# Performance work log

Hardware: AMD Instinct MI355X
Metric: run time of the kernel (lower is better)

Reference implementation:

```python
import jax, jax.numpy as jnp
import numpy as np

EPS = 1e-3        # Sinkhorn regularization (SinkhornDistance default)
MAX_ITER = 10     # max Sinkhorn iterations
THRESH = 0.1      # early-stop threshold on |u - u_prev|
N, P, D = 8, 2048, 64


def _l2norm(x):
    # F.normalize(x, dim=-1): x / max(||x||_2, 1e-12)
    return x / jnp.maximum(jnp.linalg.norm(x, axis=-1, keepdims=True), 1e-12)


def _l1norm(x):
    # F.normalize(x, p=1, dim=-1)
    return x / jnp.maximum(jnp.sum(jnp.abs(x), axis=-1, keepdims=True), 1e-12)


def _M(C, u, v):
    # modified cost M_ij = (-C_ij + u_i + v_j) / eps
    return (-C + u[..., :, None] + v[..., None, :]) / EPS


def _sinkhorn_uv(C, mu, nu):
    """Log-domain Sinkhorn with early stopping (matches torch loop + err.item() break)."""
    u0 = jnp.zeros_like(mu)
    v0 = jnp.zeros_like(nu)

    def cond(st):
        i, u, v, err = st
        return jnp.logical_and(i < MAX_ITER, err >= THRESH)

    def body(st):
        i, u, v, _ = st
        u1 = u
        u = EPS * (jnp.log(mu + 1e-8) - jax.nn.logsumexp(_M(C, u, v), axis=-1)) + u
        # logsumexp of M^T over last dim == logsumexp of M over axis -2
        v = EPS * (jnp.log(nu + 1e-8) - jax.nn.logsumexp(_M(C, u, v), axis=-2)) + v
        err = jnp.mean(jnp.sum(jnp.abs(u - u1), axis=-1))
        return (i + 1, u, v, err)

    _, u, v, _ = jax.lax.while_loop(
        cond, body, (jnp.int32(0), u0, v0, jnp.float32(jnp.inf)))
    return u, v


def setup_inputs() -> dict:
    key = jax.random.key(0)
    ka, kb = jax.random.split(key)
    a = jax.random.normal(ka, (N, P, D), dtype=jnp.float32)
    b = jax.random.normal(kb, (N, P, D), dtype=jnp.float32)
    return {"a": a, "b": b}


def reference(a, b):
    a = _l2norm(a)
    b = _l2norm(b)
    cost = 1.0 - jnp.einsum('bnd,bmd->bnm', a, b)          # [N, P1, P2]

    # weights computed from detached cost
    Cd = jax.lax.stop_gradient(cost)
    S = 1.0 - Cd
    wa = _l1norm(jnp.clip(_l1norm(jnp.mean(S, axis=2)), 0.0))  # [N, P1]
    wb = _l1norm(jnp.clip(_l1norm(jnp.mean(S, axis=1)), 0.0))  # [N, P2]

    u, v = _sinkhorn_uv(Cd, wa, wb)
    pi = jax.lax.stop_gradient(jnp.exp(_M(Cd, u, v)))       # transport plan, detached
    D_out = jnp.sum(pi * cost, axis=(-2, -1))               # [N], reduction='none'
    return D_out
```

## Files before the change

kernel.cpp:

```cpp
#include <hip/hip_runtime.h>
#include <math.h>

#define NB 8
#define PP 2048
#define DD 64
#define EPSF 1e-3f
#define RCPE 1000.0f
#define TMAX 10
#define THRESHF 0.1f
#define NEG_INF (-1e30f)
#define QSCALE 32767.5f
#define S_DEQ  (1.0f / 32767.5f)
#define KR 512
#define KC 512
#define TSEL 0.15f
#define TSELQ 4915

typedef __attribute__((ext_vector_type(8))) short bf16x8;
typedef __attribute__((ext_vector_type(4))) float f32x4;

__device__ __forceinline__ float waveAllMax(float v) {
#pragma unroll
    for (int m = 1; m < 64; m <<= 1) v = fmaxf(v, __shfl_xor(v, m, 64));
    return v;
}
__device__ __forceinline__ int waveAllMinI(int v) {
#pragma unroll
    for (int m = 1; m < 64; m <<= 1) v = min(v, __shfl_xor(v, m, 64));
    return v;
}
__device__ __forceinline__ float waveAllSum(float v) {
#pragma unroll
    for (int m = 1; m < 64; m <<= 1) v += __shfl_xor(v, m, 64);
    return v;
}
__device__ __forceinline__ short f2bf(float x) {
    unsigned b = __float_as_uint(x);
    return (short)((b + 0x7FFFu + ((b >> 16) & 1u)) >> 16);
}
__device__ __forceinline__ float bf2f(short h) {
    return __uint_as_float(((unsigned)(unsigned short)h) << 16);
}
__device__ __forceinline__ unsigned pknorm_u16(float a, float b) {
    unsigned r;
    asm("v_cvt_pknorm_u16_f32 %0, %1, %2" : "=v"(r) : "v"(a), "v"(b));
    return r;
}

__global__ void norm_kernel(const float* __restrict__ a, const float* __restrict__ b,
                            short* __restrict__ ahi, short* __restrict__ alo,
                            short* __restrict__ bhi, short* __restrict__ blo,
                            float* __restrict__ u, float* __restrict__ v,
                            int* __restrict__ conv, float* __restrict__ out,
                            float* __restrict__ Sa) {
    int gt = blockIdx.x * 256 + threadIdx.x;
    if (gt < NB * PP) { u[gt] = 0.0f; v[gt] = 0.0f; }
    if (gt == 0) *conv = 0;
    if (gt < NB) out[gt] = 0.0f;
    if (gt < 2 * NB * DD) Sa[gt] = 0.0f;
    int wave = gt >> 6;
    int lane = threadIdx.x & 63;
    const float* src; short* dhi; short* dlo; int row;
    if (wave < NB * PP) { src = a; dhi = ahi; dlo = alo; row = wave; }
    else                { src = b; dhi = bhi; dlo = blo; row = wave - NB * PP; }
    float x = src[(size_t)row * DD + lane];
    float ss = waveAllSum(x * x);
    float r = 1.0f / fmaxf(sqrtf(ss), 1e-12f);
    float xn = x * r;
    short h = f2bf(xn);
    dhi[(size_t)row * DD + lane] = h;
    dlo[(size_t)row * DD + lane] = f2bf(xn - bf2f(h));
}

__global__ void sumvec_kernel(const short* __restrict__ ahi, const short* __restrict__ alo,
                              const short* __restrict__ bhi, const short* __restrict__ blo,
                              float* __restrict__ Sa, float* __restrict__ Sb) {
    int b = blockIdx.x >> 3;
    bool isB = (blockIdx.x >> 2) & 1;
    int qtr = blockIdx.x & 3;
    const short* hi = (isB ? bhi : ahi) + ((size_t)b * PP + qtr * 512) * DD;
    const short* lo = (isB ? blo : alo) + ((size_t)b * PP + qtr * 512) * DD;
    float* dst = (isB ? Sb : Sa) + b * DD;
    int t = threadIdx.x;
    int w = t >> 6, lane = t & 63;
    int rl = lane >> 3, dq = lane & 7;
    float s[8] = {};
#pragma unroll
    for (int it = 0; it < 16; ++it) {
        size_t o = (size_t)(w * 128 + it * 8 + rl) * DD + dq * 8;
        bf16x8 h = *(const bf16x8*)(hi + o);
        bf16x8 l = *(const bf16x8*)(lo + o);
#pragma unroll
        for (int e = 0; e < 8; ++e) s[e] += bf2f(h[e]) + bf2f(l[e]);
    }
#pragma unroll
    for (int e = 0; e < 8; ++e) {
#pragma unroll
        for (int m = 8; m < 64; m <<= 1) s[e] += __shfl_xor(s[e], m, 64);
    }
    __shared__ float sh[4][64];
    if (rl == 0) {
#pragma unroll
        for (int e = 0; e < 8; ++e) sh[w][dq * 8 + e] = s[e];
    }
    __syncthreads();
    if (t < 64) atomicAdd(&dst[t], sh[0][t] + sh[1][t] + sh[2][t] + sh[3][t]);
}

__global__ __launch_bounds__(256, 4) void cost_kernel(const short* __restrict__ ahi,
        const short* __restrict__ alo, const short* __restrict__ bhi,
        const short* __restrict__ blo, unsigned short* __restrict__ C16,
        unsigned* __restrict__ rminp, unsigned* __restrict__ cminp) {
    __shared__ short Bs[2][128 * 64];
    __shared__ unsigned cmin2[4][128];
    int b  = blockIdx.z;
    int i0 = blockIdx.y * 128;
    int j0 = blockIdx.x * 128;
    int t = threadIdx.x, w = t >> 6, lane = t & 63;
    int quad = lane >> 4, li = lane & 15;
    const char* bh = (const char*)(bhi + ((size_t)b * PP + j0) * DD);
    const char* bl = (const char*)(blo + ((size_t)b * PP + j0) * DD);
    uint4 st[8];
#pragma unroll
    for (int i = 0; i < 4; ++i) {
        unsigned x = (unsigned)(t + i * 256) * 16;
        unsigned sx = x ^ (((x >> 7) & 7u) << 4);
        st[i]     = *(const uint4*)(bh + sx);
        st[4 + i] = *(const uint4*)(bl + sx);
    }
#pragma unroll
    for (int i = 0; i < 4; ++i) {
        unsigned x = (unsigned)(t + i * 256) * 16;
        *(uint4*)((char*)&Bs[0][0] + x) = st[i];
        *(uint4*)((char*)&Bs[1][0] + x) = st[4 + i];
    }
    __syncthreads();
    size_t Aoff = ((size_t)b * PP + i0 + w * 32) * DD;
    f32x4 acc[2][2][4] = {};
#pragma unroll
    for (int kc = 0; kc < 2; ++kc) {
        int k0 = kc * 32 + quad * 8;
        bf16x8 fah[2], fal[2];
#pragma unroll
        for (int mt = 0; mt < 2; ++mt) {
            size_t o = Aoff + (size_t)(mt * 16 + li) * DD + k0;
            fah[mt] = *(const bf16x8*)(ahi + o);
            fal[mt] = *(const bf16x8*)(alo + o);
        }
#pragma unroll
        for (int nh = 0; nh < 2; ++nh) {
#pragma unroll
            for (int ntl = 0; ntl < 4; ++ntl) {
                int col = nh * 64 + li * 4 + ntl;
                unsigned xo = ((unsigned)col * 128 + (unsigned)(kc * 4 + quad) * 16)
                              ^ (((unsigned)col & 7u) << 4);
                bf16x8 fbh = *(const bf16x8*)((const char*)&Bs[0][0] + xo);
                bf16x8 fbl = *(const bf16x8*)((const char*)&Bs[1][0] + xo);
#pragma unroll
                for (int mt = 0; mt < 2; ++mt) {
                    acc[mt][nh][ntl] = __builtin_amdgcn_mfma_f32_16x16x32_bf16(
                            fah[mt], fbh, acc[mt][nh][ntl], 0, 0, 0);
                    acc[mt][nh][ntl] = __builtin_amdgcn_mfma_f32_16x16x32_bf16(
                            fah[mt], fbl, acc[mt][nh][ntl], 0, 0, 0);
                    acc[mt][nh][ntl] = __builtin_amdgcn_mfma_f32_16x16x32_bf16(
                            fal[mt], fbh, acc[mt][nh][ntl], 0, 0, 0);
                }
            }
        }
    }
    unsigned cmin[2][4] = {{0xFFFFFFFFu, 0xFFFFFFFFu, 0xFFFFFFFFu, 0xFFFFFFFFu},
                           {0xFFFFFFFFu, 0xFFFFFFFFu, 0xFFFFFFFFu, 0xFFFFFFFFu}};
#pragma unroll
    for (int mt = 0; mt < 2; ++mt) {
#pragma unroll
        for (int r = 0; r < 4; ++r) {
            int irow = w * 32 + mt * 16 + quad * 4 + r;
            unsigned rm = 0xFFFFFFFFu;
            unsigned rowkey = (unsigned)(i0 + irow);
#pragma unroll
            for (int nh = 0; nh < 2; ++nh) {
                float f0 = fmaf(acc[mt][nh][0][r], -0.5f, 0.5f);
                float f1 = fmaf(acc[mt][nh][1][r], -0.5f, 0.5f);
                float f2 = fmaf(acc[mt][nh][2][r], -0.5f, 0.5f);
                float f3 = fmaf(acc[mt][nh][3][r], -0.5f, 0.5f);
                unsigned w0 = pknorm_u16(f0, f1);
                unsigned w1 = pknorm_u16(f2, f3);
                uint2 pv; pv.x = w0; pv.y = w1;
                *(uint2*)&C16[((size_t)b * PP + i0 + irow) * PP + j0 + nh * 64 + li * 4] = pv;
                unsigned colb = (unsigned)(j0 + nh * 64 + li * 4);
                unsigned lo0 = w0 << 16, hi0 = w0 & 0xFFFF0000u;
                unsigned lo1 = w1 << 16, hi1 = w1 & 0xFFFF0000u;
                rm = min(rm, min(min(lo0 | colb, hi0 | (colb + 1)),
                                 min(lo1 | (colb + 2), hi1 | (colb + 3))));
                cmin[nh][0] = min(cmin[nh][0], lo0 | rowkey);
                cmin[nh][1] = min(cmin[nh][1], hi0 | rowkey);
                cmin[nh][2] = min(cmin[nh][2], lo1 | rowkey);
                cmin[nh][3] = min(cmin[nh][3], hi1 | rowkey);
            }
#pragma unroll
            for (int m = 1; m < 16; m <<= 1)
                rm = min(rm, (unsigned)__shfl_xor((int)rm, m, 64));
            if (li == 0)
                rminp[(size_t)blockIdx.x * (NB * PP) + b * PP + i0 + irow] = rm;
        }
    }
#pragma unroll
    for (int nh = 0; nh < 2; ++nh) {
#pragma unroll
        for (int ntl = 0; ntl < 4; ++ntl) {
            unsigned cmv = cmin[nh][ntl];
            cmv = min(cmv, (unsigned)__shfl_xor((int)cmv, 16, 64));
            cmv = min(cmv, (unsigned)__shfl_xor((int)cmv, 32, 64));
            if (quad == 0) cmin2[w][nh * 64 + li * 4 + ntl] = cmv;
        }
    }
    __syncthreads();
    if (t < 128)
        cminp[(size_t)blockIdx.y * (NB * PP) + b * PP + j0 + t] =
            min(min(cmin2[0][t], cmin2[1][t]), min(cmin2[2][t], cmin2[3][t]));
}

__global__ void combine_kernel(const unsigned* __restrict__ rminp,
                               const unsigned* __restrict__ cminp,
                               unsigned* __restrict__ rowminp, unsigned* __restrict__ colminp) {
    int idx = blockIdx.x * 256 + threadIdx.x;
    unsigned rm = 0xFFFFFFFFu, cm = 0xFFFFFFFFu;
#pragma unroll
    for (int k = 0; k < 16; ++k)
        rm = min(rm, rminp[(size_t)k * (NB * PP) + idx]);
#pragma unroll
    for (int k = 0; k < 16; ++k)
        cm = min(cm, cminp[(size_t)k * (NB * PP) + idx]);
    rowminp[idx] = rm; colminp[idx] = cm;
}

__device__ __forceinline__ float blockReduceSum256(float v, float* sh) {
    v = waveAllSum(v);
    int lane = threadIdx.x & 63, w = threadIdx.x >> 6;
    if (lane == 0) sh[w] = v;
    __syncthreads();
    float r = sh[0] + sh[1] + sh[2] + sh[3];
    __syncthreads();
    return r;
}

__global__ void weights_kernel(const float* __restrict__ Sa, const float* __restrict__ Sb,
                               const short* __restrict__ ahi, const short* __restrict__ alo,
                               const short* __restrict__ bhi, const short* __restrict__ blo,
                               const unsigned* __restrict__ rowminp, const unsigned* __restrict__ colminp,
                               float* __restrict__ elm, float* __restrict__ eln,
                               unsigned short* __restrict__ rowminq,
                               unsigned short* __restrict__ colminq,
                               unsigned short* __restrict__ cthq) {
    __shared__ float sh[4];
    __shared__ float sv[64];
    int b = blockIdx.x & 7;
    bool isB = blockIdx.x >= 8;
    const short* hi = (isB ? bhi : ahi) + (size_t)b * PP * DD;
    const short* lo = (isB ? blo : alo) + (size_t)b * PP * DD;
    const float* svecg = (isB ? Sa : Sb) + b * DD;
    float* dst = (isB ? eln : elm) + b * PP;
    int tid = threadIdx.x;
    if (tid < 64) sv[tid] = svecg[tid];
    __syncthreads();
    float x[8];
    float sabs = 0.0f;
#pragma unroll
    for (int q = 0; q < 8; ++q) {
        int row = tid + q * 256;
        float dot = 0.0f;
#pragma unroll
        for (int dq = 0; dq < 8; ++dq) {
            bf16x8 h = *(const bf16x8*)(hi + (size_t)row * DD + dq * 8);
            bf16x8 l = *(const bf16x8*)(lo + (size_t)row * DD + dq * 8);
#pragma unroll
            for (int e = 0; e < 8; ++e)
                dot += (bf2f(h[e]) + bf2f(l[e])) * sv[dq * 8 + e];
        }
        x[q] = dot * (1.0f / (float)PP);
        sabs += fabsf(x[q]);
    }
    sabs = blockReduceSum256(sabs, sh);
    float inv1 = 1.0f / fmaxf(sabs, 1e-12f);
    float spos = 0.0f;
#pragma unroll
    for (int q = 0; q < 8; ++q) {
        x[q] = fmaxf(x[q] * inv1, 0.0f);
        spos += x[q];
    }
    spos = blockReduceSum256(spos, sh);
    float inv2 = 1.0f / fmaxf(spos, 1e-12f);
#pragma unroll
    for (int q = 0; q < 8; ++q)
        dst[tid + q * 256] = EPSF * logf(x[q] * inv2 + 1e-8f);
    if (isB) {
#pragma unroll
        for (int q = 0; q < 8; ++q) {
            int idx = b * PP + tid + q * 256;
            unsigned pc = colminp[idx];
            unsigned arg = pc & 0xffffu;
            unsigned pr = rowminp[b * PP + arg];
            colminq[idx] = (unsigned short)(pc >> 16);
            cthq[idx] = (unsigned short)((pc >> 16) - (pr >> 16));
        }
    } else {
#pragma unroll
        for (int q = 0; q < 8; ++q) {
            int idx = b * PP + tid + q * 256;
            rowminq[idx] = (unsigned short)(rowminp[idx] >> 16);
        }
    }
}

__global__ __launch_bounds__(256) void select_kernel(const unsigned short* __restrict__ C16,
        const unsigned short* __restrict__ colminq, const unsigned short* __restrict__ rowminq,
        const unsigned short* __restrict__ cthq,
        unsigned* __restrict__ rlist, int* __restrict__ rcnt,
        unsigned* __restrict__ clist, int* __restrict__ scnt) {
    __shared__ unsigned tile32[64][36];
    __shared__ int rm_s[64];
    __shared__ unsigned lcnt[64];
    if (blockIdx.x < 4096) {
        int w = threadIdx.x >> 6, lane = threadIdx.x & 63;
        int row = blockIdx.x * 4 + w;
        int b = row >> 11;
        const uint4* cp = (const uint4*)(C16 + (size_t)row * PP);
        uint4 q4[4];
#pragma unroll
        for (int g = 0; g < 4; ++g) q4[g] = cp[g * 64 + lane];
        const unsigned short* cmb = colminq + b * PP;
        int d[32];
        int rpmin = 0x7FFFFFFF;
#pragma unroll
        for (int g = 0; g < 4; ++g) {
            int jb = g * 512 + lane * 8;
            uint4 cmw = *(const uint4*)(cmb + jb);
            unsigned cw[4] = {cmw.x, cmw.y, cmw.z, cmw.w};
            unsigned qq[4] = {q4[g].x, q4[g].y, q4[g].z, q4[g].w};
#pragma unroll
            for (int h = 0; h < 4; ++h) {
                int d0 = (int)(qq[h] & 0xffffu) - (int)(cw[h] & 0xffffu);
                int d1 = (int)(qq[h] >> 16)     - (int)(cw[h] >> 16);
                d[g * 8 + h * 2]     = d0;
                d[g * 8 + h * 2 + 1] = d1;
                rpmin = min(rpmin, min(d0, d1));
            }
        }
        int rth = waveAllMinI(rpmin) + TSELQ;
        int cnt = 0;
#pragma unroll
        for (int e = 0; e < 32; ++e) cnt += (d[e] <= rth) ? 1 : 0;
        int inc = cnt;
#pragma unroll
        for (int m = 1; m < 64; m <<= 1) {
            int t2 = __shfl_up(inc, m, 64);
            if (lane >= m) inc += t2;
        }
        int p = inc - cnt;
        unsigned* rl = rlist + (size_t)row * KR;
#pragma unroll
        for (int g = 0; g < 4; ++g) {
            int jb = g * 512 + lane * 8;
            unsigned qq[4] = {q4[g].x, q4[g].y, q4[g].z, q4[g].w};
#pragma unroll
            for (int e = 0; e < 8; ++e) {
                if (d[g * 8 + e] <= rth) {
                    unsigned q = (qq[e >> 1] >> ((e & 1) * 16)) & 0xffffu;
                    if (p < KR) rl[p] = ((unsigned)(jb + e) << 16) | q;
                    ++p;
                }
            }
        }
        if (lane == 63) rcnt[row] = inc;
    } else {
        int bid = blockIdx.x - 4096;
        int b = bid >> 7;
        int rem = bid & 127;
        int j0 = (rem >> 2) * 64;
        int r0 = (rem & 3) * 512;
        int qq = rem & 3;
        int t = threadIdx.x;
        int col = t & 63, seg = t >> 6;
        int ctj = (int)cthq[b * PP + j0 + col] + TSELQ;
        unsigned* mylist = clist + ((size_t)(b * PP + j0 + col)) * KC + qq * 128;
        if (t < 64) lcnt[t] = 0;
        int lrow = t >> 3, lcc = t & 7;
        uint4 pf0, pf1; int pfr = 0;
        {
            const unsigned short* base0 = C16 + ((size_t)b * PP + r0 + lrow) * PP + j0;
            pf0 = ((const uint4*)base0)[lcc];
            pf1 = ((const uint4*)(base0 + (size_t)32 * PP))[lcc];
            if (t < 64) pfr = (int)rowminq[b * PP + r0 + t];
        }
        for (int chunk = 0; chunk < 8; ++chunk) {
            *(uint4*)&tile32[lrow][lcc * 4]      = pf0;
            *(uint4*)&tile32[32 + lrow][lcc * 4] = pf1;
            if (t < 64) rm_s[t] = pfr;
            __syncthreads();
            if (chunk < 7) {
                int rn = r0 + (chunk + 1) * 64;
                const unsigned short* base0 = C16 + ((size_t)b * PP + rn + lrow) * PP + j0;
                pf0 = ((const uint4*)base0)[lcc];
                pf1 = ((const uint4*)(base0 + (size_t)32 * PP))[lcc];
                if (t < 64) pfr = (int)rowminq[b * PP + rn + t];
            }
            int rbase = r0 + chunk * 64;
            unsigned qv[16];
            unsigned mask16 = 0;
            int sel = 0;
#pragma unroll
            for (int rr = 0; rr < 16; ++rr) {
                int rowl = seg * 16 + rr;
                unsigned w32 = tile32[rowl][col >> 1];
                unsigned q = (col & 1) ? (w32 >> 16) : (w32 & 0xffffu);
                qv[rr] = q;
                if ((int)q - rm_s[rowl] <= ctj) { mask16 |= 1u << rr; ++sel; }
            }
            unsigned basep = sel ? atomicAdd(&lcnt[col], (unsigned)sel) : 0u;
#pragma unroll
            for (int rr = 0; rr < 16; ++rr) {
                if (mask16 & (1u << rr)) {
                    if (basep < 128)
                        mylist[basep] = ((unsigned)(rbase + seg * 16 + rr) << 16) | qv[rr];
                    ++basep;
                }
            }
            __syncthreads();
        }
        if (t < 64)
            scnt[(b * PP + j0 + t) * 4 + qq] = min((int)lcnt[t], 128);
    }
}

__global__ __launch_bounds__(512) void u_kernel(const unsigned* __restrict__ rlist,
        const int* __restrict__ rcnt, const float* __restrict__ v,
        const float* __restrict__ elm, float* __restrict__ u, float* __restrict__ du,
        const int* __restrict__ conv) {
    if (*conv) return;
    int w = threadIdx.x >> 6, lane = threadIdx.x & 63;
    int row = blockIdx.x * 8 + w;
    int b = row >> 11;
    int cnt = min(rcnt[row], KR);
    const uint4* lst4 = (const uint4*)(rlist + (size_t)row * KR);
    const float* vb = v + (b << 11);
    int base = lane * 8;
    uint4 e0 = {0, 0, 0, 0}, e1 = {0, 0, 0, 0};
    if (base < cnt)     e0 = lst4[lane * 2];
    if (base + 4 < cnt) e1 = lst4[lane * 2 + 1];
    unsigned ev[8] = {e0.x, e0.y, e0.z, e0.w, e1.x, e1.y, e1.z, e1.w};
    float x[8];
    float m = NEG_INF;
#pragma unroll
    for (int k = 0; k < 8; ++k) {
        x[k] = NEG_INF;
        if (base + k < cnt) {
            unsigned wd = ev[k];
            x[k] = vb[wd >> 16] - (float)(wd & 0xffffu) * S_DEQ;
        }
        m = fmaxf(m, x[k]);
    }
    m = waveAllMax(m);
    float s = 0.0f;
#pragma unroll
    for (int k = 0; k < 8; ++k) s += __expf((x[k] - m) * RCPE);
    s = waveAllSum(s);
    if (lane == 0) {
        float un = elm[row] - m - EPSF * logf(s);
        du[row] = fabsf(un - u[row]);
        u[row] = un;
    }
}

__global__ __launch_bounds__(512) void v_kernel(const unsigned* __restrict__ clist,
        const int* __restrict__ scnt, const float* __restrict__ u,
        const float* __restrict__ eln, float* __restrict__ v,
        const float* __restrict__ du, int* __restrict__ conv) {
    if (*conv) return;
    int w = threadIdx.x >> 6, lane = threadIdx.x & 63;
    int jg = blockIdx.x * 8 + w;
    int b = jg >> 11;
    int4 sc = *(const int4*)&scnt[jg * 4];
    int sg = lane >> 4;
    int cn = (sg & 2) ? ((sg & 1) ? sc.w : sc.z) : ((sg & 1) ? sc.y : sc.x);
    int k0 = (lane & 15) * 8;
    const uint4* lst4 = (const uint4*)(clist + (size_t)jg * KC);
    const float* ub = u + (b << 11);
    uint4 e0 = {0, 0, 0, 0}, e1 = {0, 0, 0, 0};
    int idx4 = sg * 32 + (lane & 15) * 2;
    if (k0 < cn)     e0 = lst4[idx4];
    if (k0 + 4 < cn) e1 = lst4[idx4 + 1];
    unsigned ev[8] = {e0.x, e0.y, e0.z, e0.w, e1.x, e1.y, e1.z, e1.w};
    float x[8];
    float m = NEG_INF;
#pragma unroll
    for (int k = 0; k < 8; ++k) {
        x[k] = NEG_INF;
        if (k0 + k < cn) {
            unsigned wd = ev[k];
            x[k] = ub[wd >> 16] - (float)(wd & 0xffffu) * S_DEQ;
        }
        m = fmaxf(m, x[k]);
    }
    m = waveAllMax(m);
    float s = 0.0f;
#pragma unroll
    for (int k = 0; k < 8; ++k) s += __expf((x[k] - m) * RCPE);
    s = waveAllSum(s);
    if (lane == 0)
        v[jg] = eln[jg] - m - EPSF * logf(s);
    if (blockIdx.x == 0) {
        __shared__ float sh[8];
        int t = threadIdx.x;
        float sacc = 0.0f;
#pragma unroll
        for (int q = 0; q < 32; ++q) sacc += du[t + q * 512];
        sacc = waveAllSum(sacc);
        if (lane == 0) sh[w] = sacc;
        __syncthreads();
        if (t == 0) {
            float tot = sh[0] + sh[1] + sh[2] + sh[3] + sh[4] + sh[5] + sh[6] + sh[7];
            if (tot * (1.0f / (float)NB) < THRESHF) *conv = 1;
        }
    }
}

__global__ __launch_bounds__(512) void emd_kernel(const unsigned* __restrict__ rlist,
        const int* __restrict__ rcnt, const float* __restrict__ u,
        const float* __restrict__ v, float* __restrict__ epart) {
    __shared__ float sh[8];
    int w = threadIdx.x >> 6, lane = threadIdx.x & 63;
    int row = blockIdx.x * 8 + w;
    int b = row >> 11;
    int cnt = min(rcnt[row], KR);
    const uint4* lst4 = (const uint4*)(rlist + (size_t)row * KR);
    const float* vb = v + (b << 11);
    float ui = u[row];
    int base = lane * 8;
    uint4 e0 = {0, 0, 0, 0}, e1 = {0, 0, 0, 0};
    if (base < cnt)     e0 = lst4[lane * 2];
    if (base + 4 < cnt) e1 = lst4[lane * 2 + 1];
    unsigned ev[8] = {e0.x, e0.y, e0.z, e0.w, e1.x, e1.y, e1.z, e1.w};
    float s = 0.0f;
#pragma unroll
    for (int k = 0; k < 8; ++k) {
        if (base + k < cnt) {
            unsigned wd = ev[k];
            float cf = (float)(wd & 0xffffu) * S_DEQ;
            s += __expf((ui + vb[wd >> 16] - cf) * RCPE) * cf;
        }
    }
    s = waveAllSum(s);
    if (lane == 0) sh[w] = s;
    __syncthreads();
    if (threadIdx.x == 0)
        epart[blockIdx.x] = sh[0] + sh[1] + sh[2] + sh[3] + sh[4] + sh[5] + sh[6] + sh[7];
}

__global__ __launch_bounds__(256) void emd_finalize(const float* __restrict__ epart,
                                                    float* __restrict__ out) {
    __shared__ float sh[4];
    int b = blockIdx.x;
    int t = threadIdx.x;
    float s = epart[b * 256 + t];
    s = blockReduceSum256(s, sh);
    if (t == 0) out[b] = s;
}

extern "C" void kernel_launch(void* const* d_in, const int* in_sizes, int n_in,
                              void* d_out, int out_size, void* d_ws, size_t ws_size,
                              hipStream_t stream) {
    const float* a = (const float*)d_in[0];
    const float* b = (const float*)d_in[1];
    float* out = (float*)d_out;

    const size_t MBs = 1024ull * 1024ull;
    char* ws = (char*)d_ws;
    unsigned short* C16 = (unsigned short*)ws;
    short* ahi   = (short*)(ws + 64 * MBs);
    short* alo   = (short*)(ws + 66 * MBs);
    short* bhi   = (short*)(ws + 68 * MBs);
    short* blo   = (short*)(ws + 70 * MBs);
    unsigned* rminp = (unsigned*)(ws + 72 * MBs);
    unsigned* cminp = (unsigned*)(ws + 74 * MBs);
    unsigned* rlist = (unsigned*)(ws + 64 * MBs);
    unsigned* clist = (unsigned*)(ws + 96 * MBs);
    char* tail = ws + 128 * MBs;
    size_t off = 0;
    const size_t szV = (size_t)NB * PP * 4;
    const size_t szH = (size_t)NB * PP * 2;
    int*   scnt    = (int*)(tail + off); off += (size_t)NB * PP * 4 * 4;
    unsigned* rowminp = (unsigned*)(tail + off); off += szV;
    unsigned* colminp = (unsigned*)(tail + off); off += szV;
    unsigned short* rowminq = (unsigned short*)(tail + off); off += szH;
    unsigned short* colminq = (unsigned short*)(tail + off); off += szH;
    unsigned short* cthq    = (unsigned short*)(tail + off); off += szH;
    float* elm     = (float*)(tail + off); off += szV;
    float* eln     = (float*)(tail + off); off += szV;
    float* u       = (float*)(tail + off); off += szV;
    float* v       = (float*)(tail + off); off += szV;
    float* du      = (float*)(tail + off); off += szV;
    int*   rcnt    = (int*)(tail + off); off += szV;
    float* Sa      = (float*)(tail + off); off += (size_t)2 * NB * DD * 4;
    float* Sb      = Sa + NB * DD;
    float* epart   = (float*)(tail + off); off += (size_t)NB * PP / 8 * 4;
    int*   conv    = (int*)(tail + off); off += 64;
    if (ws_size < 128 * MBs + off) return;

    norm_kernel<<<(2 * NB * PP) / 4, 256, 0, stream>>>(a, b, ahi, alo, bhi, blo,
            u, v, conv, out, Sa);
    sumvec_kernel<<<64, 256, 0, stream>>>(ahi, alo, bhi, blo, Sa, Sb);
    cost_kernel<<<dim3(PP / 128, PP / 128, NB), 256, 0, stream>>>(
            ahi, alo, bhi, blo, C16, rminp, cminp);
    combine_kernel<<<64, 256, 0, stream>>>(rminp, cminp, rowminp, colminp);
    weights_kernel<<<16, 256, 0, stream>>>(Sa, Sb, ahi, alo, bhi, blo,
            rowminp, colminp, elm, eln, rowminq, colminq, cthq);
    select_kernel<<<4096 + 1024, 256, 0, stream>>>(C16, colminq, rowminq,
            cthq, rlist, rcnt, clist, scnt);
    for (int it = 0; it < TMAX; ++it) {
        u_kernel<<<NB * PP / 8, 512, 0, stream>>>(rlist, rcnt, v, elm, u, du, conv);
        v_kernel<<<NB * PP / 8, 512, 0, stream>>>(clist, scnt, u, eln, v, du, conv);
    }
    emd_kernel<<<NB * PP / 8, 512, 0, stream>>>(rlist, rcnt, u, v, epart);
    emd_finalize<<<NB, 256, 0, stream>>>(epart, out);
}
```

Baseline: 342.8 us.

## Process sparse Sinkhorn rows with 16-lane groups instead of full waves

The u, v and emd kernels now assign one 16-lane group per row or column instead of a 64-lane wave. Each group loops over the variable-length candidate list and reduces with 16-wide shuffles, and the grid shrinks by a factor of four. The aim is to cut idle lanes and launch overhead when candidate counts are small, at the cost of scalar, non-vectorized list loads and two passes over the list in place of register-cached values. The emd partial buffer and finalize kernel are resized to match the smaller grid.

Result: slower. 351.1 us (+2.4%).

```diff
diff --git a/kernel.cpp b/kernel.cpp
--- a/kernel.cpp
+++ b/kernel.cpp
@@ -437,34 +437,28 @@
         const float* __restrict__ elm, float* __restrict__ u, float* __restrict__ du,
         const int* __restrict__ conv) {
     if (*conv) return;
-    int w = threadIdx.x >> 6, lane = threadIdx.x & 63;
-    int row = blockIdx.x * 8 + w;
+    int g = threadIdx.x >> 4, l = threadIdx.x & 15;
+    int row = blockIdx.x * 32 + g;
     int b = row >> 11;
     int cnt = min(rcnt[row], KR);
-    const uint4* lst4 = (const uint4*)(rlist + (size_t)row * KR);
+    const unsigned* lst = rlist + (size_t)row * KR;
     const float* vb = v + (b << 11);
-    int base = lane * 8;
-    uint4 e0 = {0, 0, 0, 0}, e1 = {0, 0, 0, 0};
-    if (base < cnt)     e0 = lst4[lane * 2];
-    if (base + 4 < cnt) e1 = lst4[lane * 2 + 1];
-    unsigned ev[8] = {e0.x, e0.y, e0.z, e0.w, e1.x, e1.y, e1.z, e1.w};
-    float x[8];
     float m = NEG_INF;
-#pragma unroll
-    for (int k = 0; k < 8; ++k) {
-        x[k] = NEG_INF;
-        if (base + k < cnt) {
-            unsigned wd = ev[k];
-            x[k] = vb[wd >> 16] - (float)(wd & 0xffffu) * S_DEQ;
-        }
-        m = fmaxf(m, x[k]);
-    }
-    m = waveAllMax(m);
+    for (int e = l; e < cnt; e += 16) {
+        unsigned wd = lst[e];
+        m = fmaxf(m, vb[wd >> 16] - (float)(wd & 0xffffu) * S_DEQ);
+    }
+#pragma unroll
+    for (int mm = 1; mm < 16; mm <<= 1) m = fmaxf(m, __shfl_xor(m, mm, 64));
     float s = 0.0f;
-#pragma unroll
-    for (int k = 0; k < 8; ++k) s += __expf((x[k] - m) * RCPE);
-    s = waveAllSum(s);
-    if (lane == 0) {
+    for (int e = l; e < cnt; e += 16) {
+        unsigned wd = lst[e];
+        float x = vb[wd >> 16] - (float)(wd & 0xffffu) * S_DEQ;
+        s += __expf((x - m) * RCPE);
+    }
+#pragma unroll
+    for (int mm = 1; mm < 16; mm <<= 1) s += __shfl_xor(s, mm, 64);
+    if (l == 0) {
         float un = elm[row] - m - EPSF * logf(s);
         du[row] = fabsf(un - u[row]);
         u[row] = un;
@@ -476,41 +470,40 @@
         const float* __restrict__ eln, float* __restrict__ v,
         const float* __restrict__ du, int* __restrict__ conv) {
     if (*conv) return;
-    int w = threadIdx.x >> 6, lane = threadIdx.x & 63;
-    int jg = blockIdx.x * 8 + w;
+    int g = threadIdx.x >> 4, l = threadIdx.x & 15;
+    int jg = blockIdx.x * 32 + g;
     int b = jg >> 11;
     int4 sc = *(const int4*)&scnt[jg * 4];
-    int sg = lane >> 4;
-    int cn = (sg & 2) ? ((sg & 1) ? sc.w : sc.z) : ((sg & 1) ? sc.y : sc.x);
-    int k0 = (lane & 15) * 8;
-    const uint4* lst4 = (const uint4*)(clist + (size_t)jg * KC);
+    int cn[4] = {sc.x, sc.y, sc.z, sc.w};
+    const unsigned* lst = clist + (size_t)jg * KC;
     const float* ub = u + (b << 11);
-    uint4 e0 = {0, 0, 0, 0}, e1 = {0, 0, 0, 0};
-    int idx4 = sg * 32 + (lane & 15) * 2;
-    if (k0 < cn)     e0 = lst4[idx4];
-    if (k0 + 4 < cn) e1 = lst4[idx4 + 1];
-    unsigned ev[8] = {e0.x, e0.y, e0.z, e0.w, e1.x, e1.y, e1.z, e1.w};
-    float x[8];
     float m = NEG_INF;
 #pragma unroll
-    for (int k = 0; k < 8; ++k) {
-        x[k] = NEG_INF;
-        if (k0 + k < cn) {
-            unsigned wd = ev[k];
-            x[k] = ub[wd >> 16] - (float)(wd & 0xffffu) * S_DEQ;
-        }
-        m = fmaxf(m, x[k]);
-    }
-    m = waveAllMax(m);
+    for (int sg = 0; sg < 4; ++sg) {
+        for (int k = l; k < cn[sg]; k += 16) {
+            unsigned wd = lst[sg * 128 + k];
+            m = fmaxf(m, ub[wd >> 16] - (float)(wd & 0xffffu) * S_DEQ);
+        }
+    }
+#pragma unroll
+    for (int mm = 1; mm < 16; mm <<= 1) m = fmaxf(m, __shfl_xor(m, mm, 64));
     float s = 0.0f;
 #pragma unroll
-    for (int k = 0; k < 8; ++k) s += __expf((x[k] - m) * RCPE);
-    s = waveAllSum(s);
-    if (lane == 0)
+    for (int sg = 0; sg < 4; ++sg) {
+        for (int k = l; k < cn[sg]; k += 16) {
+            unsigned wd = lst[sg * 128 + k];
+            float x = ub[wd >> 16] - (float)(wd & 0xffffu) * S_DEQ;
+            s += __expf((x - m) * RCPE);
+        }
+    }
+#pragma unroll
+    for (int mm = 1; mm < 16; mm <<= 1) s += __shfl_xor(s, mm, 64);
+    if (l == 0)
         v[jg] = eln[jg] - m - EPSF * logf(s);
     if (blockIdx.x == 0) {
         __shared__ float sh[8];
         int t = threadIdx.x;
+        int w = t >> 6, lane = t & 63;
         float sacc = 0.0f;
 #pragma unroll
         for (int q = 0; q < 32; ++q) sacc += du[t + q * 512];
@@ -528,42 +521,33 @@
         const int* __restrict__ rcnt, const float* __restrict__ u,
         const float* __restrict__ v, float* __restrict__ epart) {
     __shared__ float sh[8];
-    int w = threadIdx.x >> 6, lane = threadIdx.x & 63;
-    int row = blockIdx.x * 8 + w;
+    int g = threadIdx.x >> 4, l = threadIdx.x & 15;
+    int row = blockIdx.x * 32 + g;
     int b = row >> 11;
     int cnt = min(rcnt[row], KR);
-    const uint4* lst4 = (const uint4*)(rlist + (size_t)row * KR);
+    const unsigned* lst = rlist + (size_t)row * KR;
     const float* vb = v + (b << 11);
     float ui = u[row];
-    int base = lane * 8;
-    uint4 e0 = {0, 0, 0, 0}, e1 = {0, 0, 0, 0};
-    if (base < cnt)     e0 = lst4[lane * 2];
-    if (base + 4 < cnt) e1 = lst4[lane * 2 + 1];
-    unsigned ev[8] = {e0.x, e0.y, e0.z, e0.w, e1.x, e1.y, e1.z, e1.w};
     float s = 0.0f;
-#pragma unroll
-    for (int k = 0; k < 8; ++k) {
-        if (base + k < cnt) {
-            unsigned wd = ev[k];
-            float cf = (float)(wd & 0xffffu) * S_DEQ;
-            s += __expf((ui + vb[wd >> 16] - cf) * RCPE) * cf;
-        }
+    for (int e = l; e < cnt; e += 16) {
+        unsigned wd = lst[e];
+        float cf = (float)(wd & 0xffffu) * S_DEQ;
+        s += __expf((ui + vb[wd >> 16] - cf) * RCPE) * cf;
     }
     s = waveAllSum(s);
+    int w = threadIdx.x >> 6, lane = threadIdx.x & 63;
     if (lane == 0) sh[w] = s;
     __syncthreads();
     if (threadIdx.x == 0)
         epart[blockIdx.x] = sh[0] + sh[1] + sh[2] + sh[3] + sh[4] + sh[5] + sh[6] + sh[7];
 }
 
-__global__ __launch_bounds__(256) void emd_finalize(const float* __restrict__ epart,
-                                                    float* __restrict__ out) {
-    __shared__ float sh[4];
-    int b = blockIdx.x;
-    int t = threadIdx.x;
-    float s = epart[b * 256 + t];
-    s = blockReduceSum256(s, sh);
-    if (t == 0) out[b] = s;
+__global__ void emd_finalize(const float* __restrict__ epart,
+                             float* __restrict__ out) {
+    int b = blockIdx.x, l = threadIdx.x;
+    float s = epart[b * 64 + l];
+    s = waveAllSum(s);
+    if (l == 0) out[b] = s;
 }
 
 extern "C" void kernel_launch(void* const* d_in, const int* in_sizes, int n_in,
@@ -602,7 +586,7 @@
     int*   rcnt    = (int*)(tail + off); off += szV;
     float* Sa      = (float*)(tail + off); off += (size_t)2 * NB * DD * 4;
     float* Sb      = Sa + NB * DD;
-    float* epart   = (float*)(tail + off); off += (size_t)NB * PP / 8 * 4;
+    float* epart   = (float*)(tail + off); off += (size_t)512 * 4;
     int*   conv    = (int*)(tail + off); off += 64;
     if (ws_size < 128 * MBs + off) return;
 
@@ -617,9 +601,9 @@
     select_kernel<<<4096 + 1024, 256, 0, stream>>>(C16, colminq, rowminq,
             cthq, rlist, rcnt, clist, scnt);
     for (int it = 0; it < TMAX; ++it) {
-        u_kernel<<<NB * PP / 8, 512, 0, stream>>>(rlist, rcnt, v, elm, u, du, conv);
-        v_kernel<<<NB * PP / 8, 512, 0, stream>>>(clist, scnt, u, eln, v, du, conv);
-    }
-    emd_kernel<<<NB * PP / 8, 512, 0, stream>>>(rlist, rcnt, u, v, epart);
-    emd_finalize<<<NB, 256, 0, stream>>>(epart, out);
-}
+        u_kernel<<<NB * PP / 32, 512, 0, stream>>>(rlist, rcnt, v, elm, u, du, conv);
+        v_kernel<<<NB * PP / 32, 512, 0, stream>>>(clist, scnt, u, eln, v, du, conv);
+    }
+    emd_kernel<<<NB * PP / 32, 512, 0, stream>>>(rlist, rcnt, u, v, epart);
+    emd_finalize<<<NB, 64, 0, stream>>>(epart, out);
+}
```
